# Performance work log

Hardware: AMD Instinct MI355X
Metric: run time of the kernel (lower is better)

## Reference

```python
import jax, jax.numpy as jnp
import numpy as np

C = 128
NUM_GROUPS = 32
EPS = 1e-6


def setup_inputs() -> dict:
    key = jax.random.key(0)
    ks = jax.random.split(key, 6)
    B, H, W = 8, 64, 64
    x = jax.random.normal(ks[0], (B, C, H, W), dtype=jnp.float32)
    # 1x1 conv weights stored as [out_c, in_c] (kernel spatial dims are 1)
    fan_avg = C  # fan_in == fan_out == C for 1x1 conv
    bound = np.sqrt(3.0 / fan_avg)
    wq = jax.random.uniform(ks[1], (C, C), jnp.float32, -bound, bound)
    wk = jax.random.uniform(ks[2], (C, C), jnp.float32, -bound, bound)
    wv = jax.random.uniform(ks[3], (C, C), jnp.float32, -bound, bound)
    # proj_out has init_scale=0.0 -> near-zero init; use tiny random instead to test math
    wo = jax.random.uniform(ks[4], (C, C), jnp.float32, -bound, bound) * 1e-3
    bq = jnp.zeros((C,), jnp.float32)
    bk = jnp.zeros((C,), jnp.float32)
    bv = jnp.zeros((C,), jnp.float32)
    bo = jnp.zeros((C,), jnp.float32)
    gamma = jnp.ones((C,), jnp.float32)
    beta = jnp.zeros((C,), jnp.float32)
    return {"x": x, "gamma": gamma, "beta": beta,
            "wq": wq, "bq": bq, "wk": wk, "bk": bk,
            "wv": wv, "bv": bv, "wo": wo, "bo": bo}


def _group_norm(x, gamma, beta):
    B, Ch, H, W = x.shape
    g = NUM_GROUPS
    xg = x.reshape(B, g, Ch // g, H, W)
    mean = jnp.mean(xg, axis=(2, 3, 4), keepdims=True)
    var = jnp.var(xg, axis=(2, 3, 4), keepdims=True)
    xn = ((xg - mean) * jax.lax.rsqrt(var + EPS)).reshape(B, Ch, H, W)
    return xn * gamma[None, :, None, None] + beta[None, :, None, None]


def _conv1x1(x, w, b):
    # x: [B,C,H,W], w: [O,C], b: [O]
    return jnp.einsum('bchw,oc->bohw', x, w) + b[None, :, None, None]


def reference(x, gamma, beta, wq, bq, wk, bk, wv, bv, wo, bo):
    B, Ch, H, W = x.shape
    n = H * W
    h = _group_norm(x, gamma, beta)
    q = _conv1x1(h, wq, bq).reshape(B, Ch, n)
    k = _conv1x1(h, wk, bk).reshape(B, Ch, n)
    v = _conv1x1(h, wv, bv).reshape(B, Ch, n)
    # attn[b, i, j] = sum_c q[b,c,i] * k[b,c,j] / sqrt(C)
    attn = jnp.einsum('bci,bcj->bij', q, k) * (float(Ch) ** -0.5)
    attn = jax.nn.softmax(attn, axis=-1)
    # h[b,c,i] = sum_j v[b,c,j] * attn[b,i,j]
    out = jnp.einsum('bcj,bij->bci', v, attn).reshape(B, Ch, H, W)
    out = _conv1x1(out, wo, bo)
    return x + out
```

## Files before the change

kernel.cpp:

```cpp
#include <hip/hip_runtime.h>


typedef float f32x4 __attribute__((ext_vector_type(4)));
typedef short short8 __attribute__((ext_vector_type(8)));
typedef _Float16 half4 __attribute__((ext_vector_type(4)));
typedef unsigned short ush;
typedef unsigned short ush4 __attribute__((ext_vector_type(4)));

__device__ __forceinline__ ush f2bf(float f) {
  unsigned u = __builtin_bit_cast(unsigned, f);
  u = (u + 0x7FFFu + ((u >> 16) & 1u)) >> 16;
  return (ush)u;
}
__device__ __forceinline__ float bf2f(ush v) {
  unsigned u = ((unsigned)v) << 16;
  return __builtin_bit_cast(float, u);
}
__device__ __forceinline__ unsigned f2fp8(float x) {
  unsigned u = __builtin_bit_cast(unsigned, x);
  unsigned s = (u >> 24) & 0x80u;
  unsigned au = u & 0x7fffffffu;
  if (au < 0x3A800000u) return s;
  if (au >= 0x43E00000u) return s | 0x7Eu;
  int e = (int)(au >> 23) - 127;
  if (e < -6) {
    float a = __builtin_bit_cast(float, au);
    int m = (int)(a * 512.0f + 0.5f);
    if (m >= 8) return s | 0x08u;
    return s | (unsigned)m;
  }
  unsigned keep = au >> 20, rem = au & 0xFFFFFu;
  keep += (rem > 0x80000u) || ((rem == 0x80000u) && (keep & 1u));
  int ef = (int)(keep >> 3) - 127;
  if (ef >= 8 && ((ef > 8) || ((keep & 7u) == 7u))) return s | 0x7Eu;
  return s | (unsigned)(((ef + 7) << 3) | (int)(keep & 7u));
}
__device__ __forceinline__ void async16(const void* g, void* l) {
  __builtin_amdgcn_global_load_lds(
      (const __attribute__((address_space(1))) unsigned int*)g,
      (__attribute__((address_space(3))) unsigned int*)l, 16, 0, 0);
}

__global__ __launch_bounds__(256) void gn_stats_kernel(
    const float* __restrict__ x, const float* __restrict__ gamma,
    const float* __restrict__ beta, float* __restrict__ scale_c,
    float* __restrict__ shift_c) {
  int bg = blockIdx.x;
  int b = bg >> 5, g = bg & 31;
  const float4* base = (const float4*)(x + (size_t)bg * 16384);
  int tid = threadIdx.x;
  float s = 0.f, sq = 0.f;
#pragma unroll
  for (int p = 0; p < 16; ++p) {
    float4 v = base[p * 256 + tid];
    s += (v.x + v.y) + (v.z + v.w);
    sq += (v.x * v.x + v.y * v.y) + (v.z * v.z + v.w * v.w);
  }
#pragma unroll
  for (int off = 32; off > 0; off >>= 1) {
    s += __shfl_down(s, off);
    sq += __shfl_down(sq, off);
  }
  __shared__ float rs[4], rq[4], mv[2];
  int w = tid >> 6, lane = tid & 63;
  if (lane == 0) { rs[w] = s; rq[w] = sq; }
  __syncthreads();
  if (tid == 0) {
    float S = (rs[0] + rs[1]) + (rs[2] + rs[3]);
    float Q = (rq[0] + rq[1]) + (rq[2] + rq[3]);
    float mean = S * (1.f / 16384.f);
    float var = Q * (1.f / 16384.f) - mean * mean;
    mv[0] = mean;
    mv[1] = rsqrtf(var + 1e-6f);
  }
  __syncthreads();
  if (tid < 4) {
    int c = (g << 2) + tid;
    float sc = mv[1] * gamma[c];
    scale_c[(b << 7) + c] = sc;
    shift_c[(b << 7) + c] = beta[c] - mv[0] * sc;
  }
}

__global__ __launch_bounds__(256) void qkv_kernel(
    const float* __restrict__ x, const float* __restrict__ scale_c,
    const float* __restrict__ shift_c, const float* __restrict__ wq,
    const float* __restrict__ wk, const float* __restrict__ wv,
    const float* __restrict__ bq, const float* __restrict__ bk,
    const float* __restrict__ bv, char* __restrict__ Qt8,
    char* __restrict__ Kt8, _Float16* __restrict__ Vh) {
  __shared__ __align__(16) ush hs[64 * 136];
  __shared__ __align__(16) ush wol[128 * 136];
  char* hs8 = (char*)hs;
  int bx = blockIdx.x;
  int type = bx >> 9;
  int rb = bx & 511;
  int b = rb >> 6, i0 = (rb & 63) << 6;
  int tid = threadIdx.x;
  int w = tid >> 6, lane = tid & 63, ln15 = lane & 15, quad = lane >> 4;

#pragma unroll
  for (int p = 0; p < 8; ++p) {
    int id = p * 256 + tid;
    int i = id & 63;
    int g8 = id >> 6;
    int c0 = g8 << 2;
    const float* xp = x + (((size_t)((b << 7) + c0)) << 12) + i0 + i;
    ush4 pk4;
#pragma unroll
    for (int e = 0; e < 4; ++e) {
      float h = xp[(size_t)e << 12] * scale_c[(b << 7) + c0 + e] +
                shift_c[(b << 7) + c0 + e];
      pk4[e] = f2bf(h);
    }
    int pg = g8 ^ ((i & 15) << 1);
    *(ush4*)(hs8 + i * 272 + pg * 8) = pk4;
  }
  const float* W = type == 0 ? wq : (type == 1 ? wk : wv);
#pragma unroll
  for (int p = 0; p < 16; ++p) {
    int v = p * 256 + tid;
    int o = v >> 5, cv = (v & 31) << 2;
    float4 w4 = *(const float4*)(W + (o << 7) + cv);
    uint2 pk;
    pk.x = (unsigned)f2bf(w4.x) | ((unsigned)f2bf(w4.y) << 16);
    pk.y = (unsigned)f2bf(w4.z) | ((unsigned)f2bf(w4.w) << 16);
    *(uint2*)&wol[o * 136 + cv] = pk;
  }
  __syncthreads();

#define HS_FRAG(row, dc) \
  (*(const short8*)(hs8 + (row) * 272 + (((((dc)*4 + quad)) ^ ((row)&15)) << 4)))

  if (type < 2) {
    f32x4 acc[8] = {};
    int hrow = w * 16 + ln15;
#pragma unroll
    for (int dc = 0; dc < 4; ++dc) {
      short8 af = HS_FRAG(hrow, dc);
#pragma unroll
      for (int nb = 0; nb < 8; ++nb) {
        short8 bf = *(const short8*)&wol[(nb * 16 + ln15) * 136 + dc * 32 + quad * 8];
        acc[nb] = __builtin_amdgcn_mfma_f32_16x16x32_bf16(af, bf, acc[nb], 0, 0, 0);
      }
    }
    const float* bias = type == 0 ? bq : bk;
    char* dst8 = type == 0 ? Qt8 : Kt8;
    __syncthreads();
#pragma unroll
    for (int nb = 0; nb < 8; ++nb) {
      int o = nb * 16 + ln15;
      float bi = bias[o];
#pragma unroll
      for (int r = 0; r < 4; ++r) {
        float val = acc[nb][r] + bi;
        if (type == 0) val *= 0.08838834764831845f;
        hs8[(w * 16 + quad * 4 + r) * 144 + o] = (char)f2fp8(val);
      }
    }
    __syncthreads();
    int i = tid >> 2, seg = tid & 3;
    uint4 d0 = *(const uint4*)(hs8 + i * 144 + seg * 32);
    uint4 d1 = *(const uint4*)(hs8 + i * 144 + seg * 32 + 16);
    char* drow = dst8 + (((size_t)((b << 12) + i0 + i)) << 7) + seg * 32;
    *(uint4*)drow = d0;
    *(uint4*)(drow + 16) = d1;
  } else {
    f32x4 acc[8] = {};
    int hrow = w * 16 + ln15;
#pragma unroll
    for (int dc = 0; dc < 4; ++dc) {
      short8 bf = HS_FRAG(hrow, dc);
#pragma unroll
      for (int mb = 0; mb < 8; ++mb) {
        short8 af = *(const short8*)&wol[(mb * 16 + ln15) * 136 + dc * 32 + quad * 8];
        acc[mb] = __builtin_amdgcn_mfma_f32_16x16x32_bf16(af, bf, acc[mb], 0, 0, 0);
      }
    }
#pragma unroll
    for (int mb = 0; mb < 8; ++mb) {
#pragma unroll
      for (int r = 0; r < 4; ++r) {
        int o = mb * 16 + quad * 4 + r;
        float val = acc[mb][r] + bv[o];
        Vh[(((size_t)((b << 7) + o)) << 12) + i0 + w * 16 + ln15] = (_Float16)val;
      }
    }
  }
#undef HS_FRAG
}

__global__ __launch_bounds__(256, 2) void attn_kernel(
    const char* __restrict__ Qt8, const char* __restrict__ Kt8,
    const _Float16* __restrict__ Vh, ush* __restrict__ po,
    float* __restrict__ lw) {
  __shared__ __align__(16) char ksb[2][4096];
  __shared__ __align__(16) _Float16 vsb[2][4096];
  int bx = blockIdx.x;
  int b = bx & 7;
  int qt = (bx >> 3) & 15;
  int ksid = bx >> 7;
  int tid = threadIdx.x;
  int w = tid >> 6, lane = tid & 63, ln15 = lane & 15, quad = lane >> 4;
  int qbase = (qt << 8) + (w << 6);
  int j0base = ksid << 10;

  long qf[4][4];
#pragma unroll
  for (int ih = 0; ih < 4; ++ih) {
    const char* qrow =
        Qt8 + (((size_t)((b << 12) + qbase + ih * 16 + ln15)) << 7);
#pragma unroll
    for (int dc = 0; dc < 4; ++dc)
      qf[ih][dc] = *(const long*)(qrow + dc * 32 + quad * 8);
  }

  int krow = (w << 3) + (lane >> 3);
  int ksg = (lane & 7) ^ (krow & 7);
  const char* ksrc =
      Kt8 + ((size_t)b << 19) + (size_t)(j0base + krow) * 128 + (ksg << 4);
  char* kdstA = &ksb[0][0] + (w << 10);
  char* kdstB = &ksb[1][0] + (w << 10);
  int vsg = (lane & 3) ^ ((lane >> 4) & 3);
  int vrow0 = (w << 5) + (lane >> 2);
  int vrow1 = vrow0 + 16;
  const _Float16* vsrc0 =
      Vh + (((size_t)((b << 7) + vrow0)) << 12) + j0base + (vsg << 3);
  const _Float16* vsrc1 =
      Vh + (((size_t)((b << 7) + vrow1)) << 12) + j0base + (vsg << 3);
  char* vdstA0 = (char*)&vsb[0][0] + ((w * 2 + 0) << 10);
  char* vdstA1 = (char*)&vsb[0][0] + ((w * 2 + 1) << 10);
  char* vdstB0 = (char*)&vsb[1][0] + ((w * 2 + 0) << 10);
  char* vdstB1 = (char*)&vsb[1][0] + ((w * 2 + 1) << 10);

  async16(ksrc, kdstA);
  async16(vsrc0, vdstA0);
  async16(vsrc1, vdstA1);
  __syncthreads();

  f32x4 O[4][8] = {};
  float lsum[4] = {0.f, 0.f, 0.f, 0.f};

  for (int jt = 0; jt < 32; ++jt) {
    int buf = jt & 1;
    if (jt + 1 < 32) {
      ksrc += 4096;
      vsrc0 += 32;
      vsrc1 += 32;
      if (buf == 0) {
        async16(ksrc, kdstB);
        async16(vsrc0, vdstB0);
        async16(vsrc1, vdstB1);
      } else {
        async16(ksrc, kdstA);
        async16(vsrc0, vdstA0);
        async16(vsrc1, vdstA1);
      }
    }
    const char* kb = &ksb[buf][0];
    const char* vb = (const char*)&vsb[buf][0];

    f32x4 S[4][2] = {};
#pragma unroll
    for (int dc = 0; dc < 4; ++dc) {
      int r0 = ln15, r1 = 16 + ln15;
      long kf0 = *(const long*)(kb + r0 * 128 +
                                ((((dc * 2 + (quad >> 1)) ^ (r0 & 7))) << 4) +
                                ((quad & 1) << 3));
      long kf1 = *(const long*)(kb + r1 * 128 +
                                ((((dc * 2 + (quad >> 1)) ^ (r1 & 7))) << 4) +
                                ((quad & 1) << 3));
#pragma unroll
      for (int ih = 0; ih < 4; ++ih) {
        S[ih][0] = __builtin_amdgcn_mfma_f32_16x16x32_fp8_fp8(kf0, qf[ih][dc], S[ih][0], 0, 0, 0);
        S[ih][1] = __builtin_amdgcn_mfma_f32_16x16x32_fp8_fp8(kf1, qf[ih][dc], S[ih][1], 0, 0, 0);
      }
    }
    half4 af[4][2];
#pragma unroll
    for (int ih = 0; ih < 4; ++ih) {
      float ls = 0.f;
#pragma unroll
      for (int mb = 0; mb < 2; ++mb) {
        float p0 = __expf(S[ih][mb][0] - 5.f);
        float p1 = __expf(S[ih][mb][1] - 5.f);
        float p2 = __expf(S[ih][mb][2] - 5.f);
        float p3 = __expf(S[ih][mb][3] - 5.f);
        ls += (p0 + p1) + (p2 + p3);
        half4 a;
        a.x = (_Float16)p0; a.y = (_Float16)p1;
        a.z = (_Float16)p2; a.w = (_Float16)p3;
        af[ih][mb] = a;
      }
      lsum[ih] += ls;
    }
#pragma unroll
    for (int nb = 0; nb < 8; ++nb) {
      int d = nb * 16 + ln15;
      int sw = (ln15 >> 2) & 3;
      const char* vrow = vb + d * 64;
      half4 vf0 = *(const half4*)(vrow + (((0 * 2 + (quad >> 1)) ^ sw) << 4) +
                                  ((quad & 1) << 3));
      half4 vf1 = *(const half4*)(vrow + (((1 * 2 + (quad >> 1)) ^ sw) << 4) +
                                  ((quad & 1) << 3));
#pragma unroll
      for (int ih = 0; ih < 4; ++ih) {
        O[ih][nb] = __builtin_amdgcn_mfma_f32_16x16x16f16(vf0, af[ih][0], O[ih][nb], 0, 0, 0);
        O[ih][nb] = __builtin_amdgcn_mfma_f32_16x16x16f16(vf1, af[ih][1], O[ih][nb], 0, 0, 0);
      }
    }
    __syncthreads();
  }

#pragma unroll
  for (int ih = 0; ih < 4; ++ih) {
    float l = lsum[ih];
    l += __shfl_xor(l, 16);
    l += __shfl_xor(l, 32);
    if (quad == 0) lw[(ksid << 15) + (b << 12) + qbase + ih * 16 + ln15] = l;
    int i = qbase + ih * 16 + ln15;
    size_t rowb = (((size_t)((ksid * 8 + b)) << 12) + i) << 7;
#pragma unroll
    for (int nb = 0; nb < 8; ++nb) {
      ush4 pk;
      pk.x = f2bf(O[ih][nb][0]);
      pk.y = f2bf(O[ih][nb][1]);
      pk.z = f2bf(O[ih][nb][2]);
      pk.w = f2bf(O[ih][nb][3]);
      *(ush4*)(po + rowb + nb * 16 + quad * 4) = pk;
    }
  }
}

__global__ __launch_bounds__(256) void proj_kernel(
    const float* __restrict__ x, const ush* __restrict__ po,
    const float* __restrict__ lw, const float* __restrict__ wo,
    const float* __restrict__ bo, float* __restrict__ out) {
  __shared__ __align__(16) ush wol[128 * 136];
  int bx = blockIdx.x;
  int b = bx >> 6, i0 = (bx & 63) << 6;
  int tid = threadIdx.x;
  int w = tid >> 6, lane = tid & 63, ln15 = lane & 15, quad = lane >> 4;
#pragma unroll
  for (int p = 0; p < 16; ++p) {
    int v = p * 256 + tid;
    int o = v >> 5, cv = (v & 31) << 2;
    float4 w4 = *(const float4*)(wo + (o << 7) + cv);
    uint2 pk;
    pk.x = (unsigned)f2bf(w4.x) | ((unsigned)f2bf(w4.y) << 16);
    pk.y = (unsigned)f2bf(w4.z) | ((unsigned)f2bf(w4.w) << 16);
    *(uint2*)&wol[o * 136 + cv] = pk;
  }
  __syncthreads();
  int iw = i0 + w * 16;
  int i = iw + ln15;
  float rl = 0.f;
#pragma unroll
  for (int s = 0; s < 4; ++s) rl += lw[(s << 15) + (b << 12) + i];
  float rinv = 1.f / rl;

  f32x4 acc[8] = {};
#pragma unroll
  for (int dc = 0; dc < 4; ++dc) {
    float vs[8] = {0.f, 0.f, 0.f, 0.f, 0.f, 0.f, 0.f, 0.f};
#pragma unroll
    for (int s = 0; s < 4; ++s) {
      short8 pv = *(const short8*)(po + (((size_t)(s * 8 + b)) << 19) +
                                   ((size_t)i << 7) + dc * 32 + quad * 8);
#pragma unroll
      for (int e = 0; e < 8; ++e) vs[e] += bf2f((ush)pv[e]);
    }
    short8 bfv;
#pragma unroll
    for (int e = 0; e < 8; ++e) bfv[e] = (short)f2bf(vs[e] * rinv);
#pragma unroll
    for (int mb = 0; mb < 8; ++mb) {
      short8 af = *(const short8*)&wol[(mb * 16 + ln15) * 136 + dc * 32 + quad * 8];
      acc[mb] = __builtin_amdgcn_mfma_f32_16x16x32_bf16(af, bfv, acc[mb], 0, 0, 0);
    }
  }
#pragma unroll
  for (int mb = 0; mb < 8; ++mb) {
#pragma unroll
    for (int r = 0; r < 4; ++r) {
      int o = mb * 16 + quad * 4 + r;
      size_t idx = (((size_t)(b << 7) + o) << 12) + i;
      out[idx] = x[idx] + acc[mb][r] + bo[o];
    }
  }
}

extern "C" void kernel_launch(void* const* d_in, const int* in_sizes, int n_in,
                              void* d_out, int out_size, void* d_ws,
                              size_t ws_size, hipStream_t stream) {
  const float* x = (const float*)d_in[0];
  const float* gamma = (const float*)d_in[1];
  const float* beta = (const float*)d_in[2];
  const float* wq = (const float*)d_in[3];
  const float* bq = (const float*)d_in[4];
  const float* wk = (const float*)d_in[5];
  const float* bk = (const float*)d_in[6];
  const float* wv = (const float*)d_in[7];
  const float* bv = (const float*)d_in[8];
  const float* wo = (const float*)d_in[9];
  const float* bo = (const float*)d_in[10];
  float* out = (float*)d_out;

  const size_t NE = (size_t)8 * 4096 * 128;
  char* Qt8 = (char*)d_ws;
  char* Kt8 = Qt8 + NE;
  _Float16* Vh = (_Float16*)(Kt8 + NE);
  ush* po = (ush*)(Vh + NE);
  float* lwp = (float*)(po + 4 * NE);
  float* scale_c = lwp + 4 * 32768;
  float* shift_c = scale_c + 1024;

  gn_stats_kernel<<<256, 256, 0, stream>>>(x, gamma, beta, scale_c, shift_c);
  qkv_kernel<<<1536, 256, 0, stream>>>(x, scale_c, shift_c, wq, wk, wv, bq, bk,
                                       bv, Qt8, Kt8, Vh);
  attn_kernel<<<512, 256, 0, stream>>>(Qt8, Kt8, Vh, po, lwp);
  proj_kernel<<<512, 256, 0, stream>>>(x, po, lwp, wo, bo, out);
}
```

Measured before the change: 204.7 us.

## Fuse output projection into attention via last-block atomic counter; use exp2 and K=32 f16 MFMA

Removes the separate proj_kernel. Each attention block bumps a per-(batch, q-tile) atomic counter after writing its partial results, and the last of the four key-split blocks runs the split reduction, output projection and residual add itself, reusing the same LDS through a union. Independently, the Q prescale now folds in log2(e) so softmax uses a raw exp2 with a shifted constant. The PV product now uses 16x16x32 f16 MFMA with half8 fragments under a new LDS swizzle for K and V. This saves a kernel launch and one pass over the partials, at the cost of a memset, fences and a serialized tail done by only a quarter of the blocks.

```diff
diff --git a/kernel.cpp b/kernel.cpp
--- a/kernel.cpp
+++ b/kernel.cpp
@@ -3,7 +3,7 @@
 
 typedef float f32x4 __attribute__((ext_vector_type(4)));
 typedef short short8 __attribute__((ext_vector_type(8)));
-typedef _Float16 half4 __attribute__((ext_vector_type(4)));
+typedef _Float16 half8 __attribute__((ext_vector_type(8)));
 typedef unsigned short ush;
 typedef unsigned short ush4 __attribute__((ext_vector_type(4)));
 
@@ -154,7 +154,7 @@
 #pragma unroll
       for (int r = 0; r < 4; ++r) {
         float val = acc[nb][r] + bi;
-        if (type == 0) val *= 0.08838834764831845f;
+        if (type == 0) val *= 0.12751742f;
         hs8[(w * 16 + quad * 4 + r) * 144 + o] = (char)f2fp8(val);
       }
     }
@@ -192,18 +192,24 @@
 
 __global__ __launch_bounds__(256, 2) void attn_kernel(
     const char* __restrict__ Qt8, const char* __restrict__ Kt8,
-    const _Float16* __restrict__ Vh, ush* __restrict__ po,
-    float* __restrict__ lw) {
-  __shared__ __align__(16) char ksb[2][4096];
-  __shared__ __align__(16) _Float16 vsb[2][4096];
+    const _Float16* __restrict__ Vh, const float* __restrict__ x,
+    const float* __restrict__ wo, const float* __restrict__ bo,
+    ush* __restrict__ po, float* __restrict__ lw, int* __restrict__ cnt,
+    float* __restrict__ out) {
+  __shared__ __align__(16) union {
+    struct {
+      char ks[2][4096];
+      _Float16 vs[2][4096];
+    } s;
+    ush wol[128 * 136];
+  } u;
+  __shared__ int winflag;
   int bx = blockIdx.x;
-  int b = bx & 7;
-  int qt = (bx >> 3) & 15;
-  int ksid = bx >> 7;
+  int b = bx & 7, qt = (bx >> 3) & 15, ksid = bx >> 7;
   int tid = threadIdx.x;
   int w = tid >> 6, lane = tid & 63, ln15 = lane & 15, quad = lane >> 4;
   int qbase = (qt << 8) + (w << 6);
-  int j0base = ksid << 10;
+  int j0 = ksid << 10;
 
   long qf[4][4];
 #pragma unroll
@@ -215,31 +221,33 @@
       qf[ih][dc] = *(const long*)(qrow + dc * 32 + quad * 8);
   }
 
-  int krow = (w << 3) + (lane >> 3);
-  int ksg = (lane & 7) ^ (krow & 7);
-  const char* ksrc =
-      Kt8 + ((size_t)b << 19) + (size_t)(j0base + krow) * 128 + (ksg << 4);
-  char* kdstA = &ksb[0][0] + (w << 10);
-  char* kdstB = &ksb[1][0] + (w << 10);
-  int vsg = (lane & 3) ^ ((lane >> 4) & 3);
-  int vrow0 = (w << 5) + (lane >> 2);
-  int vrow1 = vrow0 + 16;
+  int kj = (w << 3) + (lane >> 3);
+  int kh = (kj & 3) | (((kj >> 3) & 1) << 2);
+  int kg = (lane & 7) ^ kh;
+  const char* ksrc = Kt8 + (((size_t)((b << 12) + j0 + kj)) << 7) + (kg << 4);
+  int d0r = (w << 5) + (lane >> 2);
+  int d1r = d0r + 16;
+  int vg0 = (lane & 3) ^ (((d0r >> 1) + (d0r >> 3)) & 3);
+  int vg1 = (lane & 3) ^ (((d1r >> 1) + (d1r >> 3)) & 3);
   const _Float16* vsrc0 =
-      Vh + (((size_t)((b << 7) + vrow0)) << 12) + j0base + (vsg << 3);
+      Vh + (((size_t)((b << 7) + d0r)) << 12) + j0 + (vg0 << 3);
   const _Float16* vsrc1 =
-      Vh + (((size_t)((b << 7) + vrow1)) << 12) + j0base + (vsg << 3);
-  char* vdstA0 = (char*)&vsb[0][0] + ((w * 2 + 0) << 10);
-  char* vdstA1 = (char*)&vsb[0][0] + ((w * 2 + 1) << 10);
-  char* vdstB0 = (char*)&vsb[1][0] + ((w * 2 + 0) << 10);
-  char* vdstB1 = (char*)&vsb[1][0] + ((w * 2 + 1) << 10);
-
-  async16(ksrc, kdstA);
-  async16(vsrc0, vdstA0);
-  async16(vsrc1, vdstA1);
+      Vh + (((size_t)((b << 7) + d1r)) << 12) + j0 + (vg1 << 3);
+  char* kd[2] = {&u.s.ks[0][0] + (w << 10), &u.s.ks[1][0] + (w << 10)};
+  char* vd0[2] = {(char*)&u.s.vs[0][0] + ((w * 2 + 0) << 10),
+                  (char*)&u.s.vs[1][0] + ((w * 2 + 0) << 10)};
+  char* vd1[2] = {(char*)&u.s.vs[0][0] + ((w * 2 + 1) << 10),
+                  (char*)&u.s.vs[1][0] + ((w * 2 + 1) << 10)};
+
+  async16(ksrc, kd[0]);
+  async16(vsrc0, vd0[0]);
+  async16(vsrc1, vd1[0]);
   __syncthreads();
 
   f32x4 O[4][8] = {};
   float lsum[4] = {0.f, 0.f, 0.f, 0.f};
+  int r0 = ((ln15 >> 2) << 3) + (ln15 & 3), r1 = r0 + 4;
+  int hr = (ln15 & 3) | (((ln15 >> 2) & 1) << 2);
 
   for (int jt = 0; jt < 32; ++jt) {
     int buf = jt & 1;
@@ -247,67 +255,49 @@
       ksrc += 4096;
       vsrc0 += 32;
       vsrc1 += 32;
-      if (buf == 0) {
-        async16(ksrc, kdstB);
-        async16(vsrc0, vdstB0);
-        async16(vsrc1, vdstB1);
-      } else {
-        async16(ksrc, kdstA);
-        async16(vsrc0, vdstA0);
-        async16(vsrc1, vdstA1);
-      }
-    }
-    const char* kb = &ksb[buf][0];
-    const char* vb = (const char*)&vsb[buf][0];
+      async16(ksrc, kd[buf ^ 1]);
+      async16(vsrc0, vd0[buf ^ 1]);
+      async16(vsrc1, vd1[buf ^ 1]);
+    }
+    const char* kb = &u.s.ks[buf][0];
+    const char* vb = (const char*)&u.s.vs[buf][0];
 
     f32x4 S[4][2] = {};
 #pragma unroll
     for (int dc = 0; dc < 4; ++dc) {
-      int r0 = ln15, r1 = 16 + ln15;
-      long kf0 = *(const long*)(kb + r0 * 128 +
-                                ((((dc * 2 + (quad >> 1)) ^ (r0 & 7))) << 4) +
-                                ((quad & 1) << 3));
-      long kf1 = *(const long*)(kb + r1 * 128 +
-                                ((((dc * 2 + (quad >> 1)) ^ (r1 & 7))) << 4) +
-                                ((quad & 1) << 3));
+      int goff = ((((dc * 2 + (quad >> 1))) ^ hr) << 4) + ((quad & 1) << 3);
+      long kf0 = *(const long*)(kb + r0 * 128 + goff);
+      long kf1 = *(const long*)(kb + r1 * 128 + goff);
 #pragma unroll
       for (int ih = 0; ih < 4; ++ih) {
         S[ih][0] = __builtin_amdgcn_mfma_f32_16x16x32_fp8_fp8(kf0, qf[ih][dc], S[ih][0], 0, 0, 0);
         S[ih][1] = __builtin_amdgcn_mfma_f32_16x16x32_fp8_fp8(kf1, qf[ih][dc], S[ih][1], 0, 0, 0);
       }
     }
-    half4 af[4][2];
+    half8 pf[4];
 #pragma unroll
     for (int ih = 0; ih < 4; ++ih) {
       float ls = 0.f;
-#pragma unroll
-      for (int mb = 0; mb < 2; ++mb) {
-        float p0 = __expf(S[ih][mb][0] - 5.f);
-        float p1 = __expf(S[ih][mb][1] - 5.f);
-        float p2 = __expf(S[ih][mb][2] - 5.f);
-        float p3 = __expf(S[ih][mb][3] - 5.f);
-        ls += (p0 + p1) + (p2 + p3);
-        half4 a;
-        a.x = (_Float16)p0; a.y = (_Float16)p1;
-        a.z = (_Float16)p2; a.w = (_Float16)p3;
-        af[ih][mb] = a;
-      }
+      half8 p;
+#pragma unroll
+      for (int t = 0; t < 2; ++t)
+#pragma unroll
+        for (int r = 0; r < 4; ++r) {
+          float pv = __builtin_amdgcn_exp2f(S[ih][t][r] - 7.2134752f);
+          ls += pv;
+          p[t * 4 + r] = (_Float16)pv;
+        }
+      pf[ih] = p;
       lsum[ih] += ls;
     }
 #pragma unroll
     for (int nb = 0; nb < 8; ++nb) {
       int d = nb * 16 + ln15;
-      int sw = (ln15 >> 2) & 3;
-      const char* vrow = vb + d * 64;
-      half4 vf0 = *(const half4*)(vrow + (((0 * 2 + (quad >> 1)) ^ sw) << 4) +
-                                  ((quad & 1) << 3));
-      half4 vf1 = *(const half4*)(vrow + (((1 * 2 + (quad >> 1)) ^ sw) << 4) +
-                                  ((quad & 1) << 3));
-#pragma unroll
-      for (int ih = 0; ih < 4; ++ih) {
-        O[ih][nb] = __builtin_amdgcn_mfma_f32_16x16x16f16(vf0, af[ih][0], O[ih][nb], 0, 0, 0);
-        O[ih][nb] = __builtin_amdgcn_mfma_f32_16x16x16f16(vf1, af[ih][1], O[ih][nb], 0, 0, 0);
-      }
+      int sd = ((d >> 1) + (d >> 3)) & 3;
+      half8 vf = *(const half8*)(vb + d * 64 + ((quad ^ sd) << 4));
+#pragma unroll
+      for (int ih = 0; ih < 4; ++ih)
+        O[ih][nb] = __builtin_amdgcn_mfma_f32_16x16x32_f16(vf, pf[ih], O[ih][nb], 0, 0, 0);
     }
     __syncthreads();
   }
@@ -330,17 +320,13 @@
       *(ush4*)(po + rowb + nb * 16 + quad * 4) = pk;
     }
   }
-}
-
-__global__ __launch_bounds__(256) void proj_kernel(
-    const float* __restrict__ x, const ush* __restrict__ po,
-    const float* __restrict__ lw, const float* __restrict__ wo,
-    const float* __restrict__ bo, float* __restrict__ out) {
-  __shared__ __align__(16) ush wol[128 * 136];
-  int bx = blockIdx.x;
-  int b = bx >> 6, i0 = (bx & 63) << 6;
-  int tid = threadIdx.x;
-  int w = tid >> 6, lane = tid & 63, ln15 = lane & 15, quad = lane >> 4;
+
+  __threadfence();
+  if (tid == 0) winflag = atomicAdd(&cnt[(b << 4) + qt], 1);
+  __syncthreads();
+  if (winflag != 3) return;
+  __threadfence();
+
 #pragma unroll
   for (int p = 0; p < 16; ++p) {
     int v = p * 256 + tid;
@@ -349,43 +335,45 @@
     uint2 pk;
     pk.x = (unsigned)f2bf(w4.x) | ((unsigned)f2bf(w4.y) << 16);
     pk.y = (unsigned)f2bf(w4.z) | ((unsigned)f2bf(w4.w) << 16);
-    *(uint2*)&wol[o * 136 + cv] = pk;
-  }
-  __syncthreads();
-  int iw = i0 + w * 16;
-  int i = iw + ln15;
-  float rl = 0.f;
-#pragma unroll
-  for (int s = 0; s < 4; ++s) rl += lw[(s << 15) + (b << 12) + i];
-  float rinv = 1.f / rl;
-
-  f32x4 acc[8] = {};
-#pragma unroll
-  for (int dc = 0; dc < 4; ++dc) {
-    float vs[8] = {0.f, 0.f, 0.f, 0.f, 0.f, 0.f, 0.f, 0.f};
-#pragma unroll
-    for (int s = 0; s < 4; ++s) {
-      short8 pv = *(const short8*)(po + (((size_t)(s * 8 + b)) << 19) +
-                                   ((size_t)i << 7) + dc * 32 + quad * 8);
-#pragma unroll
-      for (int e = 0; e < 8; ++e) vs[e] += bf2f((ush)pv[e]);
-    }
-    short8 bfv;
-#pragma unroll
-    for (int e = 0; e < 8; ++e) bfv[e] = (short)f2bf(vs[e] * rinv);
+    *(uint2*)&u.wol[o * 136 + cv] = pk;
+  }
+  __syncthreads();
+
+  int iw0 = (qt << 8) + (w << 6);
+  for (int ic = 0; ic < 4; ++ic) {
+    int i = iw0 + ic * 16 + ln15;
+    float rl = 0.f;
+#pragma unroll
+    for (int s = 0; s < 4; ++s) rl += lw[(s << 15) + (b << 12) + i];
+    float rinv = 1.f / rl;
+    f32x4 acc[8] = {};
+#pragma unroll
+    for (int dc = 0; dc < 4; ++dc) {
+      float vsum[8] = {0.f, 0.f, 0.f, 0.f, 0.f, 0.f, 0.f, 0.f};
+#pragma unroll
+      for (int s = 0; s < 4; ++s) {
+        short8 pv = *(const short8*)(po + (((size_t)(s * 8 + b)) << 19) +
+                                     ((size_t)i << 7) + dc * 32 + quad * 8);
+#pragma unroll
+        for (int e = 0; e < 8; ++e) vsum[e] += bf2f((ush)pv[e]);
+      }
+      short8 bfv;
+#pragma unroll
+      for (int e = 0; e < 8; ++e) bfv[e] = (short)f2bf(vsum[e] * rinv);
+#pragma unroll
+      for (int mb = 0; mb < 8; ++mb) {
+        short8 af = *(const short8*)&u.wol[(mb * 16 + ln15) * 136 + dc * 32 + quad * 8];
+        acc[mb] = __builtin_amdgcn_mfma_f32_16x16x32_bf16(af, bfv, acc[mb], 0, 0, 0);
+      }
+    }
 #pragma unroll
     for (int mb = 0; mb < 8; ++mb) {
-      short8 af = *(const short8*)&wol[(mb * 16 + ln15) * 136 + dc * 32 + quad * 8];
-      acc[mb] = __builtin_amdgcn_mfma_f32_16x16x32_bf16(af, bfv, acc[mb], 0, 0, 0);
-    }
-  }
-#pragma unroll
-  for (int mb = 0; mb < 8; ++mb) {
-#pragma unroll
-    for (int r = 0; r < 4; ++r) {
-      int o = mb * 16 + quad * 4 + r;
-      size_t idx = (((size_t)(b << 7) + o) << 12) + i;
-      out[idx] = x[idx] + acc[mb][r] + bo[o];
+#pragma unroll
+      for (int r = 0; r < 4; ++r) {
+        int o = mb * 16 + quad * 4 + r;
+        size_t idx = (((size_t)((b << 7) + o)) << 12) + i;
+        out[idx] = x[idx] + acc[mb][r] + bo[o];
+      }
     }
   }
 }
@@ -414,10 +402,12 @@
   float* lwp = (float*)(po + 4 * NE);
   float* scale_c = lwp + 4 * 32768;
   float* shift_c = scale_c + 1024;
-
+  int* cnt = (int*)(shift_c + 1024);
+
+  (void)hipMemsetAsync(cnt, 0, 128 * sizeof(int), stream);
   gn_stats_kernel<<<256, 256, 0, stream>>>(x, gamma, beta, scale_c, shift_c);
   qkv_kernel<<<1536, 256, 0, stream>>>(x, scale_c, shift_c, wq, wk, wv, bq, bk,
                                        bv, Qt8, Kt8, Vh);
-  attn_kernel<<<512, 256, 0, stream>>>(Qt8, Kt8, Vh, po, lwp);
-  proj_kernel<<<512, 256, 0, stream>>>(x, po, lwp, wo, bo, out);
-}
+  attn_kernel<<<512, 256, 0, stream>>>(Qt8, Kt8, Vh, x, wo, bo, po, lwp, cnt,
+                                       out);
+}
```

After: 328.9 us. 60.7% more time.
